# Performance work log

Hardware: AMD Instinct MI355X
Metric: run time of the kernel (lower is better)

## Reference

```python
import jax, jax.numpy as jnp
from jax import lax
import numpy as np

N = 128      # number of dictionary atoms (ConvTranspose in_channels)
K = 16       # kernel size
S = 8        # stride
R_LR = 0.1   # SGD lr on codes R
LMDA = 0.005 # soft-threshold level
MAX_ITER = 20  # cap on ISTA iterations (torch loop is uncapped)


def conv_t(R, W):
    """torch ConvTranspose2d(N,1,K,stride=S,bias=False) with weight W[N,1,K,K].
    Implemented as a fractionally-strided conv: transpose to OIHW and flip spatial."""
    Wt = jnp.flip(jnp.transpose(W, (1, 0, 2, 3)), axis=(2, 3))  # [1,N,K,K]
    return lax.conv_general_dilated(
        R, Wt,
        window_strides=(1, 1),
        padding=[(K - 1, K - 1), (K - 1, K - 1)],
        lhs_dilation=(S, S),
        dimension_numbers=("NCHW", "OIHW", "NCHW"),
    )  # [B,1,D,D] with D=(c-1)*S+K


def ista(img, W):
    B, D = img.shape[0], img.shape[2]
    c = (D - K) // S + 1
    R0 = jnp.zeros((B, N, c, c), img.dtype)

    loss_grad = jax.grad(lambda r: jnp.sum((img - conv_t(r, W)) ** 2))

    def cond(state):
        _, i, converged = state
        return jnp.logical_and(jnp.logical_not(converged), i < MAX_ITER)

    def body(state):
        R, i, _ = state
        g = loss_grad(R)                       # dL/dR
        Rn = R - R_LR * g                      # SGD step
        Rn = jax.nn.relu(Rn - LMDA) - jax.nn.relu(-Rn - LMDA)  # soft threshold
        converged = jnp.linalg.norm(Rn - R) / jnp.linalg.norm(R) < 0.01
        return (Rn, i + 1, converged)

    R, _, _ = lax.while_loop(cond, body, (R0, jnp.int32(0), jnp.bool_(False)))
    return R


def setup_inputs() -> dict:
    key = jax.random.key(0)
    k1, k2 = jax.random.split(key)
    img = jax.random.normal(k1, (128, 1, 128, 128), jnp.float32)
    W = jax.random.normal(k2, (N, 1, K, K), jnp.float32)
    # normalize_weights(): unit L2 norm per atom (flatten over out_ch,K,K)
    W = W / jnp.linalg.norm(W.reshape(N, -1), axis=1).reshape(N, 1, 1, 1)
    return {"img_batch": img, "U_weight": W}


def reference(img_batch, U_weight):
    R = ista(img_batch, U_weight)
    return conv_t(R, U_weight)
```

## Files before the change

kernel.cpp:

```cpp
#include <hip/hip_runtime.h>
#include <stdint.h>

#define BATCH 128
#define NAT   128
#define DIM   128
#define CP    17
#define MAXIT 20
#define STEP  0.2f
#define LMD   0.005f
#define NGRAD 900

typedef short bf16x8 __attribute__((ext_vector_type(8)));
typedef float f32x16 __attribute__((ext_vector_type(16)));

#define SZ_RP (BATCH*CP*CP*NAT)
#define SZ_RS (BATCH*DIM*DIM)
#define O_RP   0
#define O_RSH  (O_RP + SZ_RP*2)
#define O_W2H  (O_RSH + SZ_RS*2)
#define O_W2L  (O_W2H + 64*512*2)
#define O_WTH  (O_W2L + 64*512*2)
#define O_WTL  (O_WTH + 128*256*2)
#define O_PART (O_WTL + 128*256*2)
#define O_FLAG (O_PART + 2048*4)

#define GLOAD16(gp, lp) __builtin_amdgcn_global_load_lds( \
    (const __attribute__((address_space(1))) uint32_t*)(gp), \
    (__attribute__((address_space(3))) uint32_t*)(lp), 16, 0, 0)

__device__ __forceinline__ void split2(float x, ushort& h, ushort& l) {
    uint32_t u = __float_as_uint(x);
    uint32_t hr = (u + 0x7FFFu + ((u >> 16) & 1u)) >> 16;
    h = (ushort)hr;
    float r = x - __uint_as_float(hr << 16);
    uint32_t u2 = __float_as_uint(r);
    l = (ushort)((u2 + 0x7FFFu + ((u2 >> 16) & 1u)) >> 16);
}
__device__ __forceinline__ float us2f(ushort u) {
    return __uint_as_float(((uint32_t)u) << 16);
}
__device__ __forceinline__ uint pk(ushort a, ushort b) {
    return (uint)a | ((uint)b << 16);
}
__device__ __forceinline__ ushort f2bf(float x) {
    uint32_t u = __float_as_uint(x);
    return (ushort)((u + 0x7FFFu + ((u >> 16) & 1u)) >> 16);
}

__global__ void kzero(uint4* __restrict__ rp, int* __restrict__ flags) {
    int i = blockIdx.x * 256 + threadIdx.x;
    rp[i] = uint4{0u, 0u, 0u, 0u};
    if (blockIdx.x == 0 && threadIdx.x < 32) flags[threadIdx.x] = 0;
}

__global__ void kprep(const float* __restrict__ W,
                      ushort* __restrict__ wth, ushort* __restrict__ wtl,
                      ushort* __restrict__ w2h, ushort* __restrict__ w2l) {
    int tid = blockIdx.x * 256 + threadIdx.x;
    int n = tid >> 8, kk = tid & 255;
    ushort h, l; split2(W[tid], h, l);
    wth[tid] = h; wtl[tid] = l;
    int kx = kk >> 4, ky = kk & 15;
    int uv = (kx & 7) * 8 + (ky & 7);
    int k2 = ((kx >> 3) * 2 + (ky >> 3)) * 128 + n;
    w2h[uv * 512 + k2] = h; w2l[uv * 512 + k2] = l;
}

__global__ void kinit0(const float* __restrict__ img, ushort* __restrict__ rsh) {
    int t8 = (blockIdx.x * 256 + threadIdx.x) * 8;
    uint hw[4];
#pragma unroll
    for (int v = 0; v < 2; ++v) {
        float4 im = *(const float4*)&img[t8 + v * 4];
        hw[v*2+0] = pk(f2bf(im.x), f2bf(im.y));
        hw[v*2+1] = pk(f2bf(im.z), f2bf(im.w));
    }
    *(uint4*)&rsh[t8] = uint4{hw[0],hw[1],hw[2],hw[3]};
}

__global__ __launch_bounds__(256) void kconvt(
    const ushort* __restrict__ rp, const ushort* __restrict__ w2h,
    const float* __restrict__ img, ushort* __restrict__ rsh,
    const float* __restrict__ partials, int* __restrict__ flags, int t)
{
    const int tid = threadIdx.x;
    {
        __shared__ float red0[16];
        __shared__ int sgate;
        float d2 = 0.f, r2 = 0.f;
        for (int i = tid; i < NGRAD; i += 256) { d2 += partials[i]; r2 += partials[1024 + i]; }
        for (int off = 32; off; off >>= 1) { d2 += __shfl_down(d2, off, 64); r2 += __shfl_down(r2, off, 64); }
        int w_ = tid >> 6, l = tid & 63;
        if (l == 0) { red0[w_] = d2; red0[8 + w_] = r2; }
        __syncthreads();
        if (tid == 0) {
            float td = red0[0] + red0[1] + red0[2] + red0[3];
            float tr = red0[8] + red0[9] + red0[10] + red0[11];
            sgate = flags[t - 1] | ((td < 1e-4f * tr) ? 1 : 0);
            if (blockIdx.x == 0) flags[t] = sgate;
        }
        __syncthreads();
        if (sgate) return;
    }

    __shared__ uint4 lds[4096];
    const int bx = blockIdx.x;
    const int bid = ((bx & 7) << 6) | (bx >> 3);
    const int m0 = bid * 64;
    const int lane = tid & 63, w = tid >> 6;
    const int wm = w >> 1, wn = w & 1, g = lane >> 5;
    const int u = (lane & 7) ^ ((lane >> 3) & 7);

    const int b0 = m0 >> 8;
    const int x0 = ((m0 & 255) >> 4) * 8;
    const int erow = tid >> 3, ec0 = (tid & 7) * 16;
    const int ebase = b0 * DIM * DIM + (x0 + erow) * DIM + ec0;
    float4 im0 = *(const float4*)&img[ebase];
    float4 im1 = *(const float4*)&img[ebase + 4];
    float4 im2 = *(const float4*)&img[ebase + 8];
    float4 im3 = *(const float4*)&img[ebase + 12];
    __builtin_amdgcn_sched_barrier(0);

    int off0[4]; const ushort* srcp[4];
#pragma unroll
    for (int i = 0; i < 4; ++i) {
        int s = w * 4 + i;
        if (s < 8) {
            int ml = s * 8 + (lane >> 3);
            int mm = m0 + ml;
            int b_ = mm >> 8, cell = mm & 255, px0 = cell >> 4, py0 = cell & 15;
            off0[i] = ((b_ * CP + px0 + 1) * CP + py0 + 1) * NAT + u * 8;
            srcp[i] = rp;
        } else {
            int ml = (s - 8) * 8 + (lane >> 3);
            off0[i] = ml * 512 + u * 8;
            srcp[i] = w2h;
        }
    }
    auto stage = [&](int kc, int buf) {
        int ij = kc >> 1;
        int dA = (kc & 1) * 64 - ((ij >> 1) * CP + (ij & 1)) * NAT;
        int dB = kc * 64;
        uint4* base = lds + buf * 1024;
#pragma unroll
        for (int i = 0; i < 4; ++i) {
            int s = w * 4 + i;
            GLOAD16(srcp[i] + off0[i] + (s < 8 ? dA : dB), base + s * 64);
        }
    };

    f32x16 acc = {};
    const int arow = wm * 32 + (lane & 31);
    const int brow = wn * 32 + (lane & 31);
    const int ax = lane & 7;

    stage(0, 0); stage(1, 1); stage(2, 2);
    for (int kc = 0; kc < 8; ++kc) {
        if (kc < 5) stage(kc + 3, (kc + 3) & 3);
        int nf = 7 - kc; nf = nf > 3 ? 3 : nf;
        switch (nf) {
            case 3: asm volatile("s_waitcnt vmcnt(12)" ::: "memory"); break;
            case 2: asm volatile("s_waitcnt vmcnt(8)"  ::: "memory"); break;
            case 1: asm volatile("s_waitcnt vmcnt(4)"  ::: "memory"); break;
            default: asm volatile("s_waitcnt vmcnt(0)" ::: "memory"); break;
        }
        __builtin_amdgcn_s_barrier();
        __builtin_amdgcn_sched_barrier(0);
        const uint4* Lb = lds + (kc & 3) * 1024;
#pragma unroll
        for (int ks = 0; ks < 4; ++ks) {
            int un = (ks * 2 + g) ^ ax;
            bf16x8 Ah = __builtin_bit_cast(bf16x8, Lb[      arow * 8 + un]);
            bf16x8 Bh = __builtin_bit_cast(bf16x8, Lb[512 + brow * 8 + un]);
            acc = __builtin_amdgcn_mfma_f32_32x32x16_bf16(Ah, Bh, acc, 0, 0, 0);
        }
        __builtin_amdgcn_sched_barrier(0);
        __builtin_amdgcn_s_barrier();
    }

    float* ldsO = (float*)lds;
    const int uvx = wn * 32 + (lane & 31);
    const int uu = uvx >> 3, vv = uvx & 7;
#pragma unroll
    for (int r = 0; r < 16; ++r) {
        int mr = m0 + wm * 32 + (r & 3) + 8 * (r >> 2) + 4 * g;
        int cl = mr & 255;
        ldsO[(((cl >> 4) & 3) * 8 + uu) * 129 + (cl & 15) * 8 + vv] = acc[r];
    }
    __syncthreads();
    const float* lrow = &ldsO[erow * 129 + ec0];
    uint hw[8];
    hw[0] = pk(f2bf(im0.x - lrow[0]),  f2bf(im0.y - lrow[1]));
    hw[1] = pk(f2bf(im0.z - lrow[2]),  f2bf(im0.w - lrow[3]));
    hw[2] = pk(f2bf(im1.x - lrow[4]),  f2bf(im1.y - lrow[5]));
    hw[3] = pk(f2bf(im1.z - lrow[6]),  f2bf(im1.w - lrow[7]));
    hw[4] = pk(f2bf(im2.x - lrow[8]),  f2bf(im2.y - lrow[9]));
    hw[5] = pk(f2bf(im2.z - lrow[10]), f2bf(im2.w - lrow[11]));
    hw[6] = pk(f2bf(im3.x - lrow[12]), f2bf(im3.y - lrow[13]));
    hw[7] = pk(f2bf(im3.z - lrow[14]), f2bf(im3.w - lrow[15]));
    *(uint4*)&rsh[ebase]     = uint4{hw[0],hw[1],hw[2],hw[3]};
    *(uint4*)&rsh[ebase + 8] = uint4{hw[4],hw[5],hw[6],hw[7]};
}

__global__ __launch_bounds__(256) void kgrad(
    const ushort* __restrict__ rsh, const ushort* __restrict__ wth,
    ushort* __restrict__ rp,
    float* __restrict__ partials, const int* __restrict__ flags, int t)
{
    if (flags[t]) return;
    __shared__ uint4 lds[3072];
    __shared__ float red0[16];
    const int tid = threadIdx.x;
    const int bx = blockIdx.x;
    const int xcd = bx & 7;
    const int bid = (xcd < 2 ? xcd * 57 : 114 + (xcd - 2) * 56) + (bx >> 3);
    const int m0 = bid * 64;
    const int n0 = blockIdx.y * 64;
    const int lane = tid & 63, w = tid >> 6;
    const int wm = w >> 1, wn = w & 1, g = lane >> 5;
    const int u = (lane & 7) ^ ((lane >> 3) & 7);

    int rbase0, rbase1; uint4 rv0, rv1;
    {
        int item = tid;
        int rowL = item >> 3, ch = item & 7;
        int mr = m0 + rowL;
        int bb = mr / 225, rm = mr % 225, pxx = rm / 15, pyy = rm % 15;
        rbase0 = ((bb * CP + pxx + 1) * CP + pyy + 1) * NAT + n0 + ch * 8;
        rv0 = *(const uint4*)&rp[rbase0];
    }
    {
        int item = 256 + tid;
        int rowL = item >> 3, ch = item & 7;
        int mr = m0 + rowL;
        int bb = mr / 225, rm = mr % 225, pxx = rm / 15, pyy = rm % 15;
        rbase1 = ((bb * CP + pxx + 1) * CP + pyy + 1) * NAT + n0 + ch * 8;
        rv1 = *(const uint4*)&rp[rbase1];
    }
    __builtin_amdgcn_sched_barrier(0);

    int off0[4]; const ushort* srcp[4];
#pragma unroll
    for (int i = 0; i < 4; ++i) {
        int s = w * 4 + i;
        if (s < 8) {
            int ml = s * 8 + (lane >> 3);
            int mA = m0 + ml, bA = mA / 225, rm = mA % 225, px = rm / 15, py = rm % 15;
            off0[i] = bA * DIM * DIM + (8 * px + (u >> 1)) * DIM + 8 * py + (u & 1) * 8;
            srcp[i] = rsh;
        } else {
            int ml = (s - 8) * 8 + (lane >> 3);
            off0[i] = (n0 + ml) * 256 + u * 8;
            srcp[i] = wth;
        }
    }
    auto stage = [&](int kc, int buf) {
        uint4* base = lds + buf * 1024;
#pragma unroll
        for (int i = 0; i < 4; ++i) {
            int s = w * 4 + i;
            GLOAD16(srcp[i] + off0[i] + (s < 8 ? kc * 512 : kc * 64), base + s * 64);
        }
    };

    f32x16 acc = {};
    const int arow = wm * 32 + (lane & 31);
    const int brow = wn * 32 + (lane & 31);
    const int ax = lane & 7;

    stage(0, 0); stage(1, 1);
    for (int kc = 0; kc < 4; ++kc) {
        if (kc < 2) stage(kc + 2, (kc + 2) % 3);
        int nf = 3 - kc; nf = nf > 2 ? 2 : nf;
        switch (nf) {
            case 2: asm volatile("s_waitcnt vmcnt(8)" ::: "memory"); break;
            case 1: asm volatile("s_waitcnt vmcnt(4)" ::: "memory"); break;
            default: asm volatile("s_waitcnt vmcnt(0)" ::: "memory"); break;
        }
        __builtin_amdgcn_s_barrier();
        __builtin_amdgcn_sched_barrier(0);
        const uint4* Lb = lds + (kc % 3) * 1024;
#pragma unroll
        for (int ks = 0; ks < 4; ++ks) {
            int un = (ks * 2 + g) ^ ax;
            bf16x8 Ah = __builtin_bit_cast(bf16x8, Lb[      arow * 8 + un]);
            bf16x8 Bh = __builtin_bit_cast(bf16x8, Lb[512 + brow * 8 + un]);
            acc = __builtin_amdgcn_mfma_f32_32x32x16_bf16(Ah, Bh, acc, 0, 0, 0);
        }
        __builtin_amdgcn_sched_barrier(0);
        __builtin_amdgcn_s_barrier();
    }

    float* ldsO = (float*)lds;
    {
        const int colL = wn * 32 + (lane & 31);
#pragma unroll
        for (int r = 0; r < 16; ++r) {
            int rowL = wm * 32 + (r & 3) + 8 * (r >> 2) + 4 * g;
            ldsO[rowL * 76 + colL] = acc[r];
        }
    }
    __syncthreads();

    float d2 = 0.f, r2 = 0.f;
#pragma unroll
    for (int i = 0; i < 2; ++i) {
        int item = i * 256 + tid;
        int rowL = item >> 3, ch = item & 7;
        uint4 hv = i ? rv1 : rv0;
        int base = i ? rbase1 : rbase0;
        const float* lp = &ldsO[rowL * 76 + ch * 8];
        uint ho[4];
#pragma unroll
        for (int wd = 0; wd < 4; ++wd) {
            uint hw_ = ((const uint*)&hv)[wd];
            ushort nh0, nh1;
            {
                float rold = us2f((ushort)hw_);
                float v = fmaf(STEP, lp[wd * 2 + 0], rold);
                float st = fmaxf(v - LMD, 0.f) - fmaxf(-v - LMD, 0.f);
                nh0 = f2bf(st);
                float df = us2f(nh0) - rold;
                d2 += df * df; r2 += rold * rold;
            }
            {
                float rold = us2f((ushort)(hw_ >> 16));
                float v = fmaf(STEP, lp[wd * 2 + 1], rold);
                float st = fmaxf(v - LMD, 0.f) - fmaxf(-v - LMD, 0.f);
                nh1 = f2bf(st);
                float df = us2f(nh1) - rold;
                d2 += df * df; r2 += rold * rold;
            }
            ho[wd] = pk(nh0, nh1);
        }
        *(uint4*)&rp[base] = uint4{ho[0], ho[1], ho[2], ho[3]};
    }

    for (int off = 32; off; off >>= 1) { d2 += __shfl_down(d2, off, 64); r2 += __shfl_down(r2, off, 64); }
    int w_ = tid >> 6, l = tid & 63;
    if (l == 0) { red0[w_] = d2; red0[8 + w_] = r2; }
    __syncthreads();
    if (tid == 0) {
        float td = red0[0] + red0[1] + red0[2] + red0[3];
        float tr = red0[8] + red0[9] + red0[10] + red0[11];
        int pb2 = blockIdx.y * 450 + bid;
        partials[pb2] = td;
        partials[1024 + pb2] = tr;
    }
}

__global__ __launch_bounds__(256) void kfinal(
    const ushort* __restrict__ rp,
    const ushort* __restrict__ w2h, const ushort* __restrict__ w2l,
    float* __restrict__ outp)
{
    const int tid = threadIdx.x;
    __shared__ uint4 lds[3072];
    const int bx = blockIdx.x;
    const int bid = ((bx & 7) << 6) | (bx >> 3);
    const int m0 = bid * 64;
    const int lane = tid & 63, w = tid >> 6;
    const int wm = w >> 1, wn = w & 1, g = lane >> 5;
    const int u = (lane & 7) ^ ((lane >> 3) & 7);

    const ushort* const srcs[3] = {rp, w2h, w2l};
    int off0[6]; const ushort* srcp[6];
#pragma unroll
    for (int i = 0; i < 6; ++i) {
        int j = w * 6 + i, p = j >> 3, jj = j & 7;
        int ml = jj * 8 + (lane >> 3);
        srcp[i] = srcs[p];
        if (p == 0) {
            int mm = m0 + ml;
            int b_ = mm >> 8, cell = mm & 255, px0 = cell >> 4, py0 = cell & 15;
            off0[i] = ((b_ * CP + px0 + 1) * CP + py0 + 1) * NAT + u * 8;
        } else {
            off0[i] = ml * 512 + u * 8;
        }
    }
    auto stage = [&](int kc, int buf) {
        int ij = kc >> 1;
        int dA = (kc & 1) * 64 - ((ij >> 1) * CP + (ij & 1)) * NAT;
        int dB = kc * 64;
#pragma unroll
        for (int i = 0; i < 6; ++i) {
            int j = w * 6 + i;
            GLOAD16(srcp[i] + off0[i] + (j < 8 ? dA : dB), lds + buf * 1536 + j * 64);
        }
    };

    f32x16 acc = {};
    const int arow = wm * 32 + (lane & 31);
    const int brow = wn * 32 + (lane & 31);
    const int ax = lane & 7;

    stage(0, 0);
    __syncthreads();
    for (int kc = 0;; ++kc) {
        const int cur = kc & 1;
        if (kc < 7) stage(kc + 1, cur ^ 1);
        const uint4* Lb = lds + cur * 1536;
#pragma unroll
        for (int ks = 0; ks < 4; ++ks) {
            int un = (ks * 2 + g) ^ ax;
            bf16x8 Ah = __builtin_bit_cast(bf16x8, Lb[       arow * 8 + un]);
            bf16x8 Bh = __builtin_bit_cast(bf16x8, Lb[512  + brow * 8 + un]);
            bf16x8 Bl = __builtin_bit_cast(bf16x8, Lb[1024 + brow * 8 + un]);
            acc = __builtin_amdgcn_mfma_f32_32x32x16_bf16(Ah, Bh, acc, 0, 0, 0);
            acc = __builtin_amdgcn_mfma_f32_32x32x16_bf16(Ah, Bl, acc, 0, 0, 0);
        }
        if (kc == 7) break;
        __syncthreads();
    }

    __syncthreads();
    float* ldsO = (float*)lds;
    const int uvx = wn * 32 + (lane & 31);
    const int uu = uvx >> 3, vv = uvx & 7;
#pragma unroll
    for (int r = 0; r < 16; ++r) {
        int mr = m0 + wm * 32 + (r & 3) + 8 * (r >> 2) + 4 * g;
        int cl = mr & 255;
        ldsO[(((cl >> 4) & 3) * 8 + uu) * 129 + (cl & 15) * 8 + vv] = acc[r];
    }
    __syncthreads();
    const int b0 = m0 >> 8;
    const int x0 = ((m0 & 255) >> 4) * 8;
    const int row = tid >> 3, c0 = (tid & 7) * 16;
    const int base = b0 * DIM * DIM + (x0 + row) * DIM + c0;
    const float* lrow = &ldsO[row * 129 + c0];
#pragma unroll
    for (int v = 0; v < 4; ++v)
        *(float4*)&outp[base + v * 4] =
            float4{lrow[v*4], lrow[v*4+1], lrow[v*4+2], lrow[v*4+3]};
}

extern "C" void kernel_launch(void* const* d_in, const int* in_sizes, int n_in,
                              void* d_out, int out_size, void* d_ws, size_t ws_size,
                              hipStream_t stream) {
    const float* img = (const float*)d_in[0];
    const float* W   = (const float*)d_in[1];
    char* ws = (char*)d_ws;
    ushort* rp  = (ushort*)(ws + O_RP);
    ushort* rsh = (ushort*)(ws + O_RSH);
    ushort* w2h = (ushort*)(ws + O_W2H);
    ushort* w2l = (ushort*)(ws + O_W2L);
    ushort* wth = (ushort*)(ws + O_WTH);
    ushort* wtl = (ushort*)(ws + O_WTL);
    float* partials = (float*)(ws + O_PART);
    int*   flags    = (int*)(ws + O_FLAG);
    float* outp = (float*)d_out;

    kzero<<<2312, 256, 0, stream>>>((uint4*)(ws + O_RP), flags);
    kprep<<<128, 256, 0, stream>>>(W, wth, wtl, w2h, w2l);
    kinit0<<<1024, 256, 0, stream>>>(img, rsh);
    kgrad<<<dim3(450, 2), 256, 0, stream>>>(rsh, wth, rp, partials, flags, 0);
    for (int t = 1; t < MAXIT; ++t) {
        kconvt<<<512, 256, 0, stream>>>(rp, w2h, img, rsh, partials, flags, t);
        kgrad<<<dim3(450, 2), 256, 0, stream>>>(rsh, wth, rp, partials, flags, t);
    }
    kfinal<<<512, 256, 0, stream>>>(rp, w2h, w2l, outp);
}
```

Baseline: 439.9 us.

## Move convergence gate into kgrad epilogue and double-buffer partials

The convergence reduction no longer runs at the start of every kconvt launch, where it serialized partial-sum loads ahead of the GEMM. kgrad now prefetches the previous iteration's partials from a double-buffered bank, reduces them after its main loop, and only commits the code update when the run has not converged. A converged state stays on by copying the old partials forward, and the flags array is removed. In exchange, kconvt and the kgrad GEMM always run, so the early-exit savings after convergence are lost.

After: 431.8 us. About the same (-1.8%).

```diff
diff --git a/kernel.cpp b/kernel.cpp
--- a/kernel.cpp
+++ b/kernel.cpp
@@ -22,7 +22,6 @@
 #define O_WTH  (O_W2L + 64*512*2)
 #define O_WTL  (O_WTH + 128*256*2)
 #define O_PART (O_WTL + 128*256*2)
-#define O_FLAG (O_PART + 2048*4)
 
 #define GLOAD16(gp, lp) __builtin_amdgcn_global_load_lds( \
     (const __attribute__((address_space(1))) uint32_t*)(gp), \
@@ -47,10 +46,9 @@
     return (ushort)((u + 0x7FFFu + ((u >> 16) & 1u)) >> 16);
 }
 
-__global__ void kzero(uint4* __restrict__ rp, int* __restrict__ flags) {
+__global__ void kzero(uint4* __restrict__ rp) {
     int i = blockIdx.x * 256 + threadIdx.x;
     rp[i] = uint4{0u, 0u, 0u, 0u};
-    if (blockIdx.x == 0 && threadIdx.x < 32) flags[threadIdx.x] = 0;
 }
 
 __global__ void kprep(const float* __restrict__ W,
@@ -80,29 +78,9 @@
 
 __global__ __launch_bounds__(256) void kconvt(
     const ushort* __restrict__ rp, const ushort* __restrict__ w2h,
-    const float* __restrict__ img, ushort* __restrict__ rsh,
-    const float* __restrict__ partials, int* __restrict__ flags, int t)
+    const float* __restrict__ img, ushort* __restrict__ rsh)
 {
     const int tid = threadIdx.x;
-    {
-        __shared__ float red0[16];
-        __shared__ int sgate;
-        float d2 = 0.f, r2 = 0.f;
-        for (int i = tid; i < NGRAD; i += 256) { d2 += partials[i]; r2 += partials[1024 + i]; }
-        for (int off = 32; off; off >>= 1) { d2 += __shfl_down(d2, off, 64); r2 += __shfl_down(r2, off, 64); }
-        int w_ = tid >> 6, l = tid & 63;
-        if (l == 0) { red0[w_] = d2; red0[8 + w_] = r2; }
-        __syncthreads();
-        if (tid == 0) {
-            float td = red0[0] + red0[1] + red0[2] + red0[3];
-            float tr = red0[8] + red0[9] + red0[10] + red0[11];
-            sgate = flags[t - 1] | ((td < 1e-4f * tr) ? 1 : 0);
-            if (blockIdx.x == 0) flags[t] = sgate;
-        }
-        __syncthreads();
-        if (sgate) return;
-    }
-
     __shared__ uint4 lds[4096];
     const int bx = blockIdx.x;
     const int bid = ((bx & 7) << 6) | (bx >> 3);
@@ -204,12 +182,11 @@
 
 __global__ __launch_bounds__(256) void kgrad(
     const ushort* __restrict__ rsh, const ushort* __restrict__ wth,
-    ushort* __restrict__ rp,
-    float* __restrict__ partials, const int* __restrict__ flags, int t)
+    ushort* __restrict__ rp, float* __restrict__ partials, int t)
 {
-    if (flags[t]) return;
     __shared__ uint4 lds[3072];
     __shared__ float red0[16];
+    __shared__ int sg;
     const int tid = threadIdx.x;
     const int bx = blockIdx.x;
     const int xcd = bx & 7;
@@ -219,7 +196,20 @@
     const int lane = tid & 63, w = tid >> 6;
     const int wm = w >> 1, wn = w & 1, g = lane >> 5;
     const int u = (lane & 7) ^ ((lane >> 3) & 7);
-
+    const int pb2 = blockIdx.y * 450 + bid;
+    const float* bankO = partials + ((t - 1) & 1) * 2048;
+    float* bankN = partials + (t & 1) * 2048;
+
+    float gd[4] = {0.f, 0.f, 0.f, 0.f}, gr[4] = {0.f, 0.f, 0.f, 0.f};
+    float pod = 0.f, por = 0.f;
+    if (t >= 1) {
+#pragma unroll
+        for (int k = 0; k < 4; ++k) {
+            int i = tid + k * 256;
+            if (i < NGRAD) { gd[k] = bankO[i]; gr[k] = bankO[1024 + i]; }
+        }
+        pod = bankO[pb2]; por = bankO[1024 + pb2];
+    }
     int rbase0, rbase1; uint4 rv0, rv1;
     {
         int item = tid;
@@ -291,6 +281,25 @@
         __builtin_amdgcn_s_barrier();
     }
 
+    int gate = 0;
+    if (t >= 1) {
+        float d2 = 0.f, r2 = 0.f;
+        d2 += gd[0]; d2 += gd[1]; d2 += gd[2]; d2 += gd[3];
+        r2 += gr[0]; r2 += gr[1]; r2 += gr[2]; r2 += gr[3];
+        for (int off = 32; off; off >>= 1) { d2 += __shfl_down(d2, off, 64); r2 += __shfl_down(r2, off, 64); }
+        int w_ = tid >> 6, l = tid & 63;
+        if (l == 0) { red0[w_] = d2; red0[8 + w_] = r2; }
+        __syncthreads();
+        if (tid == 0) {
+            float td = red0[0] + red0[1] + red0[2] + red0[3];
+            float tr = red0[8] + red0[9] + red0[10] + red0[11];
+            sg = (td < 1e-4f * tr) ? 1 : 0;
+        }
+        __syncthreads();
+        gate = sg;
+    }
+    const bool dow = (t == 0) || (gate == 0);
+
     float* ldsO = (float*)lds;
     {
         const int colL = wn * 32 + (lane & 31);
@@ -303,37 +312,39 @@
     __syncthreads();
 
     float d2 = 0.f, r2 = 0.f;
-#pragma unroll
-    for (int i = 0; i < 2; ++i) {
-        int item = i * 256 + tid;
-        int rowL = item >> 3, ch = item & 7;
-        uint4 hv = i ? rv1 : rv0;
-        int base = i ? rbase1 : rbase0;
-        const float* lp = &ldsO[rowL * 76 + ch * 8];
-        uint ho[4];
-#pragma unroll
-        for (int wd = 0; wd < 4; ++wd) {
-            uint hw_ = ((const uint*)&hv)[wd];
-            ushort nh0, nh1;
-            {
-                float rold = us2f((ushort)hw_);
-                float v = fmaf(STEP, lp[wd * 2 + 0], rold);
-                float st = fmaxf(v - LMD, 0.f) - fmaxf(-v - LMD, 0.f);
-                nh0 = f2bf(st);
-                float df = us2f(nh0) - rold;
-                d2 += df * df; r2 += rold * rold;
+    if (dow) {
+#pragma unroll
+        for (int i = 0; i < 2; ++i) {
+            int item = i * 256 + tid;
+            int rowL = item >> 3, ch = item & 7;
+            uint4 hv = i ? rv1 : rv0;
+            int base = i ? rbase1 : rbase0;
+            const float* lp = &ldsO[rowL * 76 + ch * 8];
+            uint ho[4];
+#pragma unroll
+            for (int wd = 0; wd < 4; ++wd) {
+                uint hw_ = ((const uint*)&hv)[wd];
+                ushort nh0, nh1;
+                {
+                    float rold = us2f((ushort)hw_);
+                    float v = fmaf(STEP, lp[wd * 2 + 0], rold);
+                    float st = fmaxf(v - LMD, 0.f) - fmaxf(-v - LMD, 0.f);
+                    nh0 = f2bf(st);
+                    float df = us2f(nh0) - rold;
+                    d2 += df * df; r2 += rold * rold;
+                }
+                {
+                    float rold = us2f((ushort)(hw_ >> 16));
+                    float v = fmaf(STEP, lp[wd * 2 + 1], rold);
+                    float st = fmaxf(v - LMD, 0.f) - fmaxf(-v - LMD, 0.f);
+                    nh1 = f2bf(st);
+                    float df = us2f(nh1) - rold;
+                    d2 += df * df; r2 += rold * rold;
+                }
+                ho[wd] = pk(nh0, nh1);
             }
-            {
-                float rold = us2f((ushort)(hw_ >> 16));
-                float v = fmaf(STEP, lp[wd * 2 + 1], rold);
-                float st = fmaxf(v - LMD, 0.f) - fmaxf(-v - LMD, 0.f);
-                nh1 = f2bf(st);
-                float df = us2f(nh1) - rold;
-                d2 += df * df; r2 += rold * rold;
-            }
-            ho[wd] = pk(nh0, nh1);
-        }
-        *(uint4*)&rp[base] = uint4{ho[0], ho[1], ho[2], ho[3]};
+            *(uint4*)&rp[base] = uint4{ho[0], ho[1], ho[2], ho[3]};
+        }
     }
 
     for (int off = 32; off; off >>= 1) { d2 += __shfl_down(d2, off, 64); r2 += __shfl_down(r2, off, 64); }
@@ -341,11 +352,15 @@
     if (l == 0) { red0[w_] = d2; red0[8 + w_] = r2; }
     __syncthreads();
     if (tid == 0) {
-        float td = red0[0] + red0[1] + red0[2] + red0[3];
-        float tr = red0[8] + red0[9] + red0[10] + red0[11];
-        int pb2 = blockIdx.y * 450 + bid;
-        partials[pb2] = td;
-        partials[1024 + pb2] = tr;
+        if (dow) {
+            float td = red0[0] + red0[1] + red0[2] + red0[3];
+            float tr = red0[8] + red0[9] + red0[10] + red0[11];
+            bankN[pb2] = td;
+            bankN[1024 + pb2] = tr;
+        } else {
+            bankN[pb2] = pod;
+            bankN[1024 + pb2] = por;
+        }
     }
 }
 
@@ -448,16 +463,15 @@
     ushort* wth = (ushort*)(ws + O_WTH);
     ushort* wtl = (ushort*)(ws + O_WTL);
     float* partials = (float*)(ws + O_PART);
-    int*   flags    = (int*)(ws + O_FLAG);
     float* outp = (float*)d_out;
 
-    kzero<<<2312, 256, 0, stream>>>((uint4*)(ws + O_RP), flags);
+    kzero<<<2312, 256, 0, stream>>>((uint4*)(ws + O_RP));
     kprep<<<128, 256, 0, stream>>>(W, wth, wtl, w2h, w2l);
     kinit0<<<1024, 256, 0, stream>>>(img, rsh);
-    kgrad<<<dim3(450, 2), 256, 0, stream>>>(rsh, wth, rp, partials, flags, 0);
+    kgrad<<<dim3(450, 2), 256, 0, stream>>>(rsh, wth, rp, partials, 0);
     for (int t = 1; t < MAXIT; ++t) {
-        kconvt<<<512, 256, 0, stream>>>(rp, w2h, img, rsh, partials, flags, t);
-        kgrad<<<dim3(450, 2), 256, 0, stream>>>(rsh, wth, rp, partials, flags, t);
+        kconvt<<<512, 256, 0, stream>>>(rp, w2h, img, rsh);
+        kgrad<<<dim3(450, 2), 256, 0, stream>>>(rsh, wth, rp, partials, t);
     }
     kfinal<<<512, 256, 0, stream>>>(rp, w2h, w2l, outp);
 }
```
